# Optimization experiments

Measured on AMD Instinct MI355X. Metric: run time of the kernel, lower is better.

## Reference

```python
import jax, jax.numpy as jnp
import numpy as np

EPS = 1e-5


def _bn_silu(x, gamma, beta):
    # train-mode BatchNorm2d (biased batch stats over N,H,W) followed by SiLU
    m = jnp.mean(x, axis=(0, 2, 3), keepdims=True)
    v = jnp.var(x, axis=(0, 2, 3), keepdims=True)
    y = gamma[None, :, None, None] * (x - m) * jax.lax.rsqrt(v + EPS) + beta[None, :, None, None]
    return y * jax.nn.sigmoid(y)


def _deform_conv2d(x, offset, w, b):
    # x: [B,C,H,W]; offset: [B,2*9,H,W] as (dy,dx) pairs per 3x3 tap; w: [Co,C,3,3]
    B, C, H, W = x.shape
    Co = w.shape[0]
    off = offset.reshape(B, 9, 2, H, W)
    k = jnp.arange(9)
    ky = (k // 3 - 1).astype(x.dtype)  # kernel tap offsets, pad=1 so centered
    kx = (k % 3 - 1).astype(x.dtype)
    py = jnp.arange(H, dtype=x.dtype)[None, None, :, None] + ky[None, :, None, None] + off[:, :, 0]
    px = jnp.arange(W, dtype=x.dtype)[None, None, None, :] + kx[None, :, None, None] + off[:, :, 1]
    y0 = jnp.floor(py)
    x0 = jnp.floor(px)
    wy1 = py - y0
    wx1 = px - x0
    xf = x.reshape(B, C, H * W)

    def corner(yi, xi, cw):
        # zero-padded bilinear corner: mask out-of-bounds taps via weight
        valid = (yi >= 0) & (yi < H) & (xi >= 0) & (xi < W)
        idx = jnp.clip(yi, 0, H - 1) * W + jnp.clip(xi, 0, W - 1)
        g = jnp.take_along_axis(xf, idx.reshape(B, 1, -1), axis=2).reshape(B, C, 9, H, W)
        return g * (cw * valid.astype(x.dtype))[:, None]

    y0i = y0.astype(jnp.int32)
    x0i = x0.astype(jnp.int32)
    s = corner(y0i, x0i, (1 - wy1) * (1 - wx1))
    s = s + corner(y0i, x0i + 1, (1 - wy1) * wx1)
    s = s + corner(y0i + 1, x0i, wy1 * (1 - wx1))
    s = s + corner(y0i + 1, x0i + 1, wy1 * wx1)
    out = jnp.einsum('bckhw,ock->bohw', s, w.reshape(Co, C, 9))
    return out + b[None, :, None, None]


def _conv_transpose(x, w, stride, pad):
    # torch ConvTranspose2d: weight layout [Cin, Cout, kh, kw]
    k = w.shape[2]
    wf = jnp.flip(w, (2, 3)).transpose(1, 0, 2, 3)  # -> OIHW, spatially flipped
    p = k - 1 - pad
    return jax.lax.conv_general_dilated(
        x, wf, (1, 1), [(p, p), (p, p)], lhs_dilation=(stride, stride),
        dimension_numbers=('NCHW', 'OIHW', 'NCHW'))


def setup_inputs() -> dict:
    key = jax.random.key(0)
    ks = jax.random.split(key, 4)
    B, C, Co, H, W = 16, 256, 256, 32, 32
    r = lambda k, s, sc: jax.random.normal(k, s, jnp.float32) * sc
    return {
        'x': r(ks[0], (B, C, H, W), 1.0),
        'w_off': r(ks[1], (18, C, 3, 3), 0.01),
        'b_off': jnp.zeros((18,), jnp.float32),
        'w_def': r(ks[2], (Co, C, 3, 3), 0.02),
        'b_def': jnp.zeros((Co,), jnp.float32),
        'gamma1': jnp.ones((Co,), jnp.float32),
        'beta1': jnp.zeros((Co,), jnp.float32),
        'w_dc': r(ks[3], (Co, Co, 4, 4), 0.02),
        'gamma2': jnp.ones((Co,), jnp.float32),
        'beta2': jnp.zeros((Co,), jnp.float32),
    }


def reference(x, w_off, b_off, w_def, b_def, gamma1, beta1, w_dc, gamma2, beta2):
    offset = jax.lax.conv_general_dilated(
        x, w_off, (1, 1), [(1, 1), (1, 1)],
        dimension_numbers=('NCHW', 'OIHW', 'NCHW')) + b_off[None, :, None, None]
    y = _deform_conv2d(x, offset, w_def, b_def)
    y = _bn_silu(y, gamma1, beta1)
    y = _conv_transpose(y, w_dc, 2, 1)
    return _bn_silu(y, gamma2, beta2)
```

## Files before the change

### kernel.cpp

```cpp
#include <hip/hip_runtime.h>
#include <math.h>

#ifdef __has_builtin
#if __has_builtin(__builtin_amdgcn_global_load_lds)
#define HAS_GLL 1
#endif
#endif
#ifndef HAS_GLL
#define HAS_GLL 0
#endif

typedef __attribute__((ext_vector_type(8))) short short8v;
typedef __attribute__((ext_vector_type(4))) float float4v;

__device__ __forceinline__ unsigned short f2bf(float f) {
    unsigned int u = __float_as_uint(f);
    u += 0x7fffu + ((u >> 16) & 1u);
    return (unsigned short)(u >> 16);
}

__device__ __forceinline__ float silu(float y) { return y / (1.f + expf(-y)); }

__device__ __forceinline__ void stage1k(const void* gsrc, void* ldsbase) {
#if HAS_GLL
    __builtin_amdgcn_global_load_lds((const __attribute__((address_space(1))) unsigned int*)gsrc,
                                     (__attribute__((address_space(3))) unsigned int*)ldsbase,
                                     16, 0, 0);
#else
    int lane = threadIdx.x & 63;
    *(float4*)((char*)ldsbase + lane * 16) = *(const float4*)gsrc;
#endif
}

__global__ __launch_bounds__(256) void k_prep_xt(const float* __restrict__ x,
                                                 unsigned short* __restrict__ xT) {
    int hw0 = blockIdx.x * 32, c0 = blockIdx.y * 32, b = blockIdx.z;
    int t = threadIdx.x;
    __shared__ unsigned short tl[32][36];
    {
        int c_l = t >> 3, w4 = (t & 7) * 4;
        float4 v = *(const float4*)&x[(size_t)((b * 256 + c0 + c_l) * 1024) + hw0 + w4];
        tl[c_l][w4 + 0] = f2bf(v.x);
        tl[c_l][w4 + 1] = f2bf(v.y);
        tl[c_l][w4 + 2] = f2bf(v.z);
        tl[c_l][w4 + 3] = f2bf(v.w);
    }
    __syncthreads();
    {
        int hw_l = t >> 3, c4 = (t & 7) * 4;
        unsigned int s0 = tl[c4 + 0][hw_l];
        unsigned int s1 = tl[c4 + 1][hw_l];
        unsigned int s2 = tl[c4 + 2][hw_l];
        unsigned int s3 = tl[c4 + 3][hw_l];
        uint2 pk;
        pk.x = s0 | (s1 << 16);
        pk.y = s2 | (s3 << 16);
        *(uint2*)&xT[(size_t)((b * 1024 + hw0 + hw_l) * 256) + c0 + c4] = pk;
    }
}

__global__ void k_prep_aoff(const float* __restrict__ w_off, unsigned short* __restrict__ A2off) {
    int i = blockIdx.x * 256 + threadIdx.x;
    int slot = i & 31;
    int oc = (i >> 5) & 31;
    int rest = i >> 10;
    int tap = rest % 9;
    int cc8 = rest / 9;
    int cgrp = (slot >> 3) ^ ((oc >> 1) & 3);
    int c = cc8 * 32 + (cgrp << 3) + (slot & 7);
    unsigned short v = 0;
    if (oc < 18) v = f2bf(w_off[(size_t)oc * 2304 + c * 9 + tap]);
    A2off[i] = v;
}

__global__ void k_prep_a1(const float* __restrict__ w_def, unsigned short* __restrict__ A1) {
    int i = blockIdx.x * 256 + threadIdx.x;
    A1[i] = f2bf(w_def[i]);
}

__global__ void k_prep_a2(const float* __restrict__ w_dc, unsigned short* __restrict__ A2) {
    int i = blockIdx.x * 256 + threadIdx.x;
    int ci = i & 255;
    int tq = (i >> 8) & 3;
    int co = (i >> 10) & 255;
    int p  = i >> 18;
    int ph = p >> 1, pw = p & 1;
    int ty = tq >> 1, tx = tq & 1;
    int kh = 2 * ty + 1 - ph;
    int kw = 2 * tx + 1 - pw;
    A2[i] = f2bf(w_dc[((ci * 256 + co) * 4 + kh) * 4 + kw]);
}

__global__ __launch_bounds__(256) void k_off_gemm(const unsigned short* __restrict__ A2off,
                                                  const unsigned short* __restrict__ xT,
                                                  const float* __restrict__ b_off,
                                                  float* __restrict__ off) {
    int hp = blockIdx.x, b = blockIdx.y;
    int h0 = hp * 2;
    int t = threadIdx.x;
    int lane = t & 63, wid = t >> 6;
    int l15 = lane & 15, g = lane >> 4;
    int swg = (l15 >> 1) & 3;
    __shared__ __align__(16) unsigned short As[9 * 32 * 32];
    __shared__ __align__(16) unsigned short Bsx[4 * 34 * 32];
    float4v acc[2];
    float4v z = {0.f, 0.f, 0.f, 0.f};
    acc[0] = z; acc[1] = z;

    int pos = wid * 16 + l15;
    int py = pos >> 5, px = pos & 31;

    for (int cc8 = 0; cc8 < 8; ++cc8) {
        __syncthreads();
        for (int idx = t; idx < 1152; idx += 256)
            stage1k(A2off + (size_t)cc8 * 9216 + idx * 8, (char*)As + idx * 16);
        for (int idx = t; idx < 544; idx += 256) {
            int r = idx / 136;
            int rem = idx - r * 136;
            int col = rem >> 2;
            int sgrp = rem & 3;
            int grp = sgrp ^ ((col >> 1) & 3);
            int h = h0 - 1 + r;
            int w = col - 1;
            uint4 v = {0u, 0u, 0u, 0u};
            if (h >= 0 && h < 32 && w >= 0 && w < 32)
                v = *(const uint4*)&xT[(size_t)((b * 1024 + h * 32 + w) * 256) + cc8 * 32 + grp * 8];
            *(uint4*)((char*)Bsx + ((r * 34 + col) << 6) + (sgrp << 4)) = v;
        }
        __syncthreads();
#pragma unroll
        for (int tap = 0; tap < 9; ++tap) {
            int ky = tap / 3, kx = tap - ky * 3;
            int col = px + kx;
            int rowr = py + ky;
            short8v bbf = *(const short8v*)((const char*)Bsx + ((rowr * 34 + col) << 6) +
                                            ((g ^ ((col >> 1) & 3)) << 4));
            short8v a0 = *(const short8v*)((const char*)As + tap * 2048 + l15 * 64 + ((g ^ swg) << 4));
            short8v a1 = *(const short8v*)((const char*)As + tap * 2048 + (16 + l15) * 64 + ((g ^ swg) << 4));
            acc[0] = __builtin_amdgcn_mfma_f32_16x16x32_bf16(a0, bbf, acc[0], 0, 0, 0);
            acc[1] = __builtin_amdgcn_mfma_f32_16x16x32_bf16(a1, bbf, acc[1], 0, 0, 0);
        }
    }
    int h = h0 + py;
#pragma unroll
    for (int r = 0; r < 4; ++r) {
        int oc = g * 4 + r;
        off[((size_t)(b * 18 + oc) << 10) + (h << 5) + px] = acc[0][r] + b_off[oc];
    }
    if (g == 0) {
#pragma unroll
        for (int r = 0; r < 2; ++r) {
            int oc = 16 + r;
            off[((size_t)(b * 18 + oc) << 10) + (h << 5) + px] = acc[1][r] + b_off[oc];
        }
    }
}

__global__ __launch_bounds__(576) void k_sample(const float* __restrict__ x,
                                                const float* __restrict__ off,
                                                unsigned short* __restrict__ S) {
    int cg = blockIdx.x, b = blockIdx.y, half = blockIdx.z;
    int cbase = cg * 8;
    int t = threadIdx.x;
    int k = t >> 6, lane = t & 63;
    __shared__ __align__(16) unsigned int xpl[4 * 1156];
    __shared__ __align__(16) unsigned short sS[72 * 66];

    for (int u = t; u < 1024; u += 576) {
        int p = u >> 8, row = (u >> 3) & 31, cq = (u & 7) << 2;
        const float* src0 = x + ((size_t)(b * 256 + cbase + 2 * p) << 10) + (row << 5) + cq;
        float4 a = *(const float4*)src0;
        float4 c = *(const float4*)(src0 + 1024);
        uint4 pk;
        pk.x = (unsigned int)f2bf(a.x) | ((unsigned int)f2bf(c.x) << 16);
        pk.y = (unsigned int)f2bf(a.y) | ((unsigned int)f2bf(c.y) << 16);
        pk.z = (unsigned int)f2bf(a.z) | ((unsigned int)f2bf(c.z) << 16);
        pk.w = (unsigned int)f2bf(a.w) | ((unsigned int)f2bf(c.w) << 16);
        *(uint4*)&xpl[p * 1156 + row * 36 + cq] = pk;
    }

    int wr_row = t / 9, wr_q = t - wr_row * 9;
    const float* offk0 = off + ((size_t)(b * 18 + 2 * k) << 10);
    const float* offk1 = off + ((size_t)(b * 18 + 2 * k + 1) << 10);
    int ky = k / 3 - 1, kx = k % 3 - 1;
    __syncthreads();

    for (int ci = 0; ci < 8; ++ci) {
        int chunk = half * 8 + ci;
        int pos = chunk * 64 + lane;
        int h = pos >> 5, w = pos & 31;
        float dy = offk0[pos];
        float dx = offk1[pos];
        float py = (float)(h + ky) + dy;
        float px = (float)(w + kx) + dx;
        float fy = floorf(py), fx = floorf(px);
        int y0i = (int)fy, x0i = (int)fx;
        float wy = py - fy, wxf = px - fx;
        float vy0 = (y0i >= 0 && y0i < 32) ? 1.f : 0.f;
        float vy1 = (y0i >= -1 && y0i < 31) ? 1.f : 0.f;
        float vx0 = (x0i >= 0 && x0i < 32) ? 1.f : 0.f;
        float vx1 = (x0i >= -1 && x0i < 31) ? 1.f : 0.f;
        int y0c = min(max(y0i, 0), 31), y1c = min(max(y0i + 1, 0), 31);
        int x0c = min(max(x0i, 0), 31), x1c = min(max(x0i + 1, 0), 31);
        float w00 = (1.f - wy) * (1.f - wxf) * vy0 * vx0;
        float w01 = (1.f - wy) * wxf * vy0 * vx1;
        float w10 = wy * (1.f - wxf) * vy1 * vx0;
        float w11 = wy * wxf * vy1 * vx1;
        int a00 = y0c * 36 + x0c, a01 = y0c * 36 + x1c;
        int a10 = y1c * 36 + x0c, a11 = y1c * 36 + x1c;
#pragma unroll
        for (int p = 0; p < 4; ++p) {
            const unsigned int* pl = xpl + p * 1156;
            unsigned int c00 = pl[a00], c01 = pl[a01], c10 = pl[a10], c11 = pl[a11];
            float e00 = __uint_as_float(c00 << 16), o00 = __uint_as_float(c00 & 0xFFFF0000u);
            float e01 = __uint_as_float(c01 << 16), o01 = __uint_as_float(c01 & 0xFFFF0000u);
            float e10 = __uint_as_float(c10 << 16), o10 = __uint_as_float(c10 & 0xFFFF0000u);
            float e11 = __uint_as_float(c11 << 16), o11 = __uint_as_float(c11 & 0xFFFF0000u);
            float ve = w00 * e00 + w01 * e01 + w10 * e10 + w11 * e11;
            float vo = w00 * o00 + w01 * o01 + w10 * o10 + w11 * o11;
            sS[((2 * p) * 9 + k) * 66 + lane] = f2bf(ve);
            sS[((2 * p + 1) * 9 + k) * 66 + lane] = f2bf(vo);
        }
        __syncthreads();
        {
            int basekc = wr_q * 8;
            unsigned int s0 = sS[(basekc + 0) * 66 + wr_row];
            unsigned int s1 = sS[(basekc + 1) * 66 + wr_row];
            unsigned int s2 = sS[(basekc + 2) * 66 + wr_row];
            unsigned int s3 = sS[(basekc + 3) * 66 + wr_row];
            unsigned int s4 = sS[(basekc + 4) * 66 + wr_row];
            unsigned int s5 = sS[(basekc + 5) * 66 + wr_row];
            unsigned int s6 = sS[(basekc + 6) * 66 + wr_row];
            unsigned int s7 = sS[(basekc + 7) * 66 + wr_row];
            uint4 qv;
            qv.x = s0 | (s1 << 16);
            qv.y = s2 | (s3 << 16);
            qv.z = s4 | (s5 << 16);
            qv.w = s6 | (s7 << 16);
            *(uint4*)(S + (size_t)(b * 1024 + chunk * 64 + wr_row) * 2304 + cg * 72 + wr_q * 8) = qv;
        }
        __syncthreads();
    }
}

__global__ __launch_bounds__(256) void k_gemm1(const unsigned short* __restrict__ A1,
                                               const unsigned short* __restrict__ S,
                                               const float* __restrict__ b_def,
                                               float* __restrict__ y1) {
    int nb = blockIdx.x, mb = blockIdx.y;
    int t = threadIdx.x;
    int lane = t & 63, wid = t >> 6;
    int wm = wid >> 1, wn = wid & 1;
    __shared__ __align__(16) unsigned short As[128 * 32];
    __shared__ __align__(16) unsigned short Bs[64 * 32];
    int m0 = mb * 128, n0 = nb * 64;
    float4v acc[4][2];
    float4v z = {0.f, 0.f, 0.f, 0.f};
#pragma unroll
    for (int i = 0; i < 4; ++i) { acc[i][0] = z; acc[i][1] = z; }
    int rQ = lane >> 2;
    int qA = (lane & 3) ^ ((lane >> 3) & 3);
    const unsigned short* gA0 = A1 + (size_t)(m0 + wid * 32 + rQ) * 2304 + qA * 8;
    const unsigned short* gA1 = gA0 + (size_t)16 * 2304;
    const unsigned short* gB0 = S + (size_t)(n0 + wid * 16 + rQ) * 2304 + qA * 8;
    unsigned short* lA0 = As + wid * 32 * 32;
    unsigned short* lA1 = As + (wid * 32 + 16) * 32;
    unsigned short* lB0 = Bs + wid * 16 * 32;
    int g = lane >> 4, l15 = lane & 15;
    int gs = (g ^ ((l15 >> 1) & 3)) << 4;
    for (int s = 0; s < 72; ++s) {
        __syncthreads();
        stage1k(gA0 + s * 32, lA0);
        stage1k(gA1 + s * 32, lA1);
        stage1k(gB0 + s * 32, lB0);
        __syncthreads();
        short8v a[4], bb[2];
#pragma unroll
        for (int mi = 0; mi < 4; ++mi)
            a[mi] = *(const short8v*)((const char*)As + ((wm * 64 + mi * 16 + l15) * 64 + gs));
#pragma unroll
        for (int ni = 0; ni < 2; ++ni)
            bb[ni] = *(const short8v*)((const char*)Bs + ((wn * 32 + ni * 16 + l15) * 64 + gs));
#pragma unroll
        for (int mi = 0; mi < 4; ++mi)
#pragma unroll
            for (int ni = 0; ni < 2; ++ni)
                acc[mi][ni] = __builtin_amdgcn_mfma_f32_16x16x32_bf16(a[mi], bb[ni], acc[mi][ni], 0, 0, 0);
    }
    int b = n0 >> 10;
    int posb = n0 & 1023;
#pragma unroll
    for (int mi = 0; mi < 4; ++mi) {
#pragma unroll
        for (int r = 0; r < 4; ++r) {
            int co = m0 + wm * 64 + mi * 16 + g * 4 + r;
            float bv = b_def[co];
            float* dst = y1 + ((size_t)(b * 256 + co) << 10) + posb;
#pragma unroll
            for (int ni = 0; ni < 2; ++ni)
                dst[wn * 32 + ni * 16 + l15] = acc[mi][ni][r] + bv;
        }
    }
}

__global__ __launch_bounds__(256) void k_gemm2(const unsigned short* __restrict__ A2,
                                               const unsigned short* __restrict__ y1T,
                                               float* __restrict__ outP,
                                               float* __restrict__ pstats2) {
    int nb = blockIdx.x, mb = blockIdx.y, p = blockIdx.z;
    int ph = p >> 1, pw = p & 1;
    int t = threadIdx.x;
    int lane = t & 63, wid = t >> 6;
    int wm = wid >> 1, wn = wid & 1;
    int l15 = lane & 15, g = lane >> 4;
    __shared__ __align__(16) unsigned short As[128 * 64];
    __shared__ __align__(16) unsigned short Bs[128 * 64];
    int m0 = mb * 128, n0 = nb * 128;
    int b = n0 >> 10, pos0 = n0 & 1023, oh0 = pos0 >> 5;

    int dtab[4];
#pragma unroll
    for (int tap = 0; tap < 4; ++tap) {
        int ty = tap >> 1, tx = tap & 1;
        int dy = ph ? (1 - ty) : (-ty);
        int dx = pw ? (1 - tx) : (-tx);
        dtab[tap] = (dy * 34 + dx) * 256;
    }
    const unsigned short* srcA[4];
    const unsigned short* srcB[4];
    unsigned short* dstA[4];
    unsigned short* dstB[4];
#pragma unroll
    for (int it = 0; it < 4; ++it) {
        int idx = t + it * 256;
        int r = idx >> 3, s8 = idx & 7, c = s8 ^ (r & 7);
        srcA[it] = A2 + (size_t)(p * 256 + m0 + r) * 1024 + c * 8;
        dstA[it] = As + idx * 8;
        int ih = oh0 + (r >> 5) + 1;
        int iw = (r & 31) + 1;
        srcB[it] = y1T + ((size_t)(b * 34 + ih) * 34 + iw) * 256 + c * 8;
        dstB[it] = Bs + idx * 8;
    }

    float4v acc[4][4];
    float4v z = {0.f, 0.f, 0.f, 0.f};
#pragma unroll
    for (int i = 0; i < 4; ++i)
#pragma unroll
        for (int j = 0; j < 4; ++j) acc[i][j] = z;

    for (int step = 0; step < 16; ++step) {
        int tap = step >> 2;
        int koff = step * 64;
        int boff = dtab[tap] + (step & 3) * 64;
        __syncthreads();
#pragma unroll
        for (int it = 0; it < 4; ++it) {
            stage1k(srcA[it] + koff, dstA[it]);
            stage1k(srcB[it] + boff, dstB[it]);
        }
        __syncthreads();
#pragma unroll
        for (int kk = 0; kk < 2; ++kk) {
            short8v a[4], bb[4];
#pragma unroll
            for (int mi = 0; mi < 4; ++mi) {
                int row = wm * 64 + mi * 16 + l15;
                int slot = ((kk << 2) + g) ^ (row & 7);
                a[mi] = *(const short8v*)((const char*)As + row * 128 + slot * 16);
            }
#pragma unroll
            for (int ni = 0; ni < 4; ++ni) {
                int row = wn * 64 + ni * 16 + l15;
                int slot = ((kk << 2) + g) ^ (row & 7);
                bb[ni] = *(const short8v*)((const char*)Bs + row * 128 + slot * 16);
            }
#pragma unroll
            for (int mi = 0; mi < 4; ++mi)
#pragma unroll
                for (int ni = 0; ni < 4; ++ni)
                    acc[mi][ni] = __builtin_amdgcn_mfma_f32_16x16x32_bf16(a[mi], bb[ni], acc[mi][ni], 0, 0, 0);
        }
    }
#pragma unroll
    for (int mi = 0; mi < 4; ++mi) {
#pragma unroll
        for (int r = 0; r < 4; ++r) {
            int co = m0 + wm * 64 + mi * 16 + g * 4 + r;
            float* dst = outP + ((size_t)((p * 16 + b) * 256 + co) << 10) + pos0;
#pragma unroll
            for (int ni = 0; ni < 4; ++ni)
                dst[wn * 64 + ni * 16 + l15] = acc[mi][ni][r];
        }
    }
    __syncthreads();
    float* sred  = (float*)As;
    float* s2red = sred + 256;
#pragma unroll
    for (int mi = 0; mi < 4; ++mi) {
#pragma unroll
        for (int r = 0; r < 4; ++r) {
            float s = 0.f, s2 = 0.f;
#pragma unroll
            for (int ni = 0; ni < 4; ++ni) {
                float v = acc[mi][ni][r];
                s += v;
                s2 += v * v;
            }
#pragma unroll
            for (int m = 8; m >= 1; m >>= 1) {
                s  += __shfl_xor(s, m, 64);
                s2 += __shfl_xor(s2, m, 64);
            }
            if (l15 == 0) {
                int col = wm * 64 + mi * 16 + g * 4 + r;
                sred[col * 2 + wn]  = s;
                s2red[col * 2 + wn] = s2;
            }
        }
    }
    __syncthreads();
    if (t < 128) {
        float s  = sred[t * 2] + sred[t * 2 + 1];
        float s2 = s2red[t * 2] + s2red[t * 2 + 1];
        int row = p * 128 + nb;
        int ch = mb * 128 + t;
        pstats2[ch * 512 + row] = s;
        pstats2[131072 + ch * 512 + row] = s2;
    }
}

__global__ __launch_bounds__(256) void k_bnstats_part(const float* __restrict__ src, int nparts,
                                                      float* __restrict__ pstats) {
    int ch = blockIdx.x, j = blockIdx.y;
    int t = threadIdx.x;
    const float* p = src + ((size_t)(j * 256 + ch) << 10);
    float4 v = *(const float4*)&p[t * 4];
    float s  = v.x + v.y + v.z + v.w;
    float s2 = v.x * v.x + v.y * v.y + v.z * v.z + v.w * v.w;
    __shared__ float rs[256], rs2[256];
    rs[t] = s; rs2[t] = s2;
    __syncthreads();
    for (int d = 128; d > 0; d >>= 1) {
        if (t < d) { rs[t] += rs[t + d]; rs2[t] += rs2[t + d]; }
        __syncthreads();
    }
    if (t == 0) {
        pstats[ch * nparts + j] = rs[0];
        pstats[256 * nparts + ch * nparts + j] = rs2[0];
    }
}

__global__ __launch_bounds__(256) void k_bnfin(const float* __restrict__ pstats, int nparts, float n,
                                               float* __restrict__ mean, float* __restrict__ rstd) {
    int ch = threadIdx.x;
    float s = 0.f, s2 = 0.f;
    for (int j = 0; j < nparts; ++j) {
        s += pstats[ch * nparts + j];
        s2 += pstats[256 * nparts + ch * nparts + j];
    }
    float m = s / n;
    float var = s2 / n - m * m;
    mean[ch] = m;
    rstd[ch] = rsqrtf(var + 1e-5f);
}

__global__ __launch_bounds__(256) void k_bnfin2(const float* __restrict__ pstats2,
                                                float* __restrict__ mean, float* __restrict__ rstd) {
    int ch = blockIdx.x;
    int t = threadIdx.x;
    float s  = pstats2[ch * 512 + t] + pstats2[ch * 512 + 256 + t];
    float s2 = pstats2[131072 + ch * 512 + t] + pstats2[131072 + ch * 512 + 256 + t];
    __shared__ float rs[256], rs2[256];
    rs[t] = s; rs2[t] = s2;
    __syncthreads();
    for (int d = 128; d > 0; d >>= 1) {
        if (t < d) { rs[t] += rs[t + d]; rs2[t] += rs2[t + d]; }
        __syncthreads();
    }
    if (t == 0) {
        float n = 65536.f;
        float m = rs[0] / n;
        float var = rs2[0] / n - m * m;
        mean[ch] = m;
        rstd[ch] = rsqrtf(var + 1e-5f);
    }
}

__global__ __launch_bounds__(256) void k_bnsilu_padT(const float* __restrict__ y1,
                                                     const float* __restrict__ mean,
                                                     const float* __restrict__ rstd,
                                                     const float* __restrict__ gamma,
                                                     const float* __restrict__ beta,
                                                     unsigned short* __restrict__ y1T) {
    int py = blockIdx.x, cg = blockIdx.y, b = blockIdx.z;
    int c0 = cg * 32;
    int t = threadIdx.x;
    __shared__ unsigned short tl[32][36];
    {
        int c_l = t >> 3, px4 = (t & 7) * 4;
        int ch = c0 + c_l;
        float m = mean[ch], rs = rstd[ch], ga = gamma[ch], be = beta[ch];
        float4 v = *(const float4*)&y1[(size_t)((b * 256 + ch) << 10) + (py << 5) + px4];
        tl[c_l][px4 + 0] = f2bf(silu(ga * (v.x - m) * rs + be));
        tl[c_l][px4 + 1] = f2bf(silu(ga * (v.y - m) * rs + be));
        tl[c_l][px4 + 2] = f2bf(silu(ga * (v.z - m) * rs + be));
        tl[c_l][px4 + 3] = f2bf(silu(ga * (v.w - m) * rs + be));
    }
    __syncthreads();
    {
        int px = t >> 3, c4 = (t & 7) * 4;
        unsigned int s0 = tl[c4 + 0][px];
        unsigned int s1 = tl[c4 + 1][px];
        unsigned int s2 = tl[c4 + 2][px];
        unsigned int s3 = tl[c4 + 3][px];
        uint2 pk;
        pk.x = s0 | (s1 << 16);
        pk.y = s2 | (s3 << 16);
        *(uint2*)&y1T[((size_t)(b * 34 + py + 1) * 34 + (px + 1)) * 256 + c0 + c4] = pk;
    }
}

__global__ __launch_bounds__(256) void k_bnsilu_out(const float* __restrict__ outP,
                                                    const float* __restrict__ mean,
                                                    const float* __restrict__ rstd,
                                                    const float* __restrict__ gamma,
                                                    const float* __restrict__ beta,
                                                    float* __restrict__ out) {
    unsigned int i = blockIdx.x * 256 + threadIdx.x;
    int ow4 = i & 15;
    int oh = (i >> 4) & 63;
    int co = (i >> 10) & 255;
    int b  = i >> 18;
    int p0 = (oh & 1) * 2;
    int pos = ((oh >> 1) << 5) + ow4 * 2;
    const float* pl0 = outP + ((size_t)((p0 * 16 + b) * 256 + co) << 10) + pos;
    const float* pl1 = pl0 + ((size_t)16 * 256 << 10);
    float2 e = *(const float2*)pl0;
    float2 o = *(const float2*)pl1;
    float m = mean[co], rs = rstd[co], ga = gamma[co], be = beta[co];
    float4 v;
    v.x = silu(ga * (e.x - m) * rs + be);
    v.y = silu(ga * (o.x - m) * rs + be);
    v.z = silu(ga * (e.y - m) * rs + be);
    v.w = silu(ga * (o.y - m) * rs + be);
    *(float4*)&out[((size_t)(b * 256 + co) << 12) + (oh << 6) + ow4 * 4] = v;
}

extern "C" void kernel_launch(void* const* d_in, const int* in_sizes, int n_in,
                              void* d_out, int out_size, void* d_ws, size_t ws_size,
                              hipStream_t stream) {
    const float* x      = (const float*)d_in[0];
    const float* w_off  = (const float*)d_in[1];
    const float* b_off  = (const float*)d_in[2];
    const float* w_def  = (const float*)d_in[3];
    const float* b_def  = (const float*)d_in[4];
    const float* gamma1 = (const float*)d_in[5];
    const float* beta1  = (const float*)d_in[6];
    const float* w_dc   = (const float*)d_in[7];
    const float* gamma2 = (const float*)d_in[8];
    const float* beta2  = (const float*)d_in[9];
    float* out = (float*)d_out;

    char* base = (char*)d_ws;
    unsigned short* S    = (unsigned short*)base;
    float*          y1   = (float*)(base + 75497472);
    unsigned short* y1T  = (unsigned short*)(base + 92274688);
    unsigned short* A1   = (unsigned short*)(base + 101744640);
    unsigned short* A2   = (unsigned short*)(base + 102924288);
    float*          off  = (float*)(base + 105021440);
    float*          stats = (float*)(base + 106201088);
    float* mean1 = stats, *rstd1 = stats + 256, *mean2 = stats + 512, *rstd2 = stats + 768;
    float* pstats = off;
    float* pstats2 = off;
    unsigned short* xT    = (unsigned short*)base;
    unsigned short* A2off = (unsigned short*)(base + 8388608);
    float* outP = (float*)base;

    k_prep_a1<<<2304, 256, 0, stream>>>(w_def, A1);
    k_prep_a2<<<4096, 256, 0, stream>>>(w_dc, A2);
    k_prep_aoff<<<288, 256, 0, stream>>>(w_off, A2off);
    k_prep_xt<<<dim3(32, 8, 16), 256, 0, stream>>>(x, xT);
    k_off_gemm<<<dim3(16, 16), 256, 0, stream>>>(A2off, xT, b_off, off);
    k_sample<<<dim3(32, 16, 2), 576, 0, stream>>>(x, off, S);
    k_gemm1<<<dim3(256, 2), 256, 0, stream>>>(A1, S, b_def, y1);
    k_bnstats_part<<<dim3(256, 16), 256, 0, stream>>>(y1, 16, pstats);
    k_bnfin<<<1, 256, 0, stream>>>(pstats, 16, 16384.f, mean1, rstd1);
    hipMemsetAsync(y1T, 0, 9469952, stream);
    k_bnsilu_padT<<<dim3(32, 8, 16), 256, 0, stream>>>(y1, mean1, rstd1, gamma1, beta1, y1T);
    k_gemm2<<<dim3(128, 2, 4), 256, 0, stream>>>(A2, y1T, outP, pstats2);
    k_bnfin2<<<256, 256, 0, stream>>>(pstats2, mean2, rstd2);
    k_bnsilu_out<<<16384, 256, 0, stream>>>(outP, mean2, rstd2, gamma2, beta2, out);
}
```

Baseline: 212.4 us.

## Double-buffer LDS in both GEMMs, enlarge gemm1 tile, fuse BN1 stats into gemm1

Both GEMM kernels now use two LDS buffers, so the next K-slice loads while MFMAs run on the current one, and each step needs one barrier instead of two. gemm1 moves from a 128x64 tile with K=32 to a 128x128 tile with K=64 and the same swizzled layout as gemm2. Its epilogue also computes per-channel partial sums and sums of squares, which removes the separate k_bnstats_part pass over y1. The cost is 64KB of LDS per block, which may lower occupancy, and k_bnfin now reduces 128 partials per channel instead of 16.

```diff
diff --git a/kernel.cpp b/kernel.cpp
--- a/kernel.cpp
+++ b/kernel.cpp
@@ -246,60 +246,114 @@
 __global__ __launch_bounds__(256) void k_gemm1(const unsigned short* __restrict__ A1,
                                                const unsigned short* __restrict__ S,
                                                const float* __restrict__ b_def,
-                                               float* __restrict__ y1) {
+                                               float* __restrict__ y1,
+                                               float* __restrict__ pstats1) {
     int nb = blockIdx.x, mb = blockIdx.y;
     int t = threadIdx.x;
     int lane = t & 63, wid = t >> 6;
     int wm = wid >> 1, wn = wid & 1;
-    __shared__ __align__(16) unsigned short As[128 * 32];
-    __shared__ __align__(16) unsigned short Bs[64 * 32];
-    int m0 = mb * 128, n0 = nb * 64;
-    float4v acc[4][2];
+    int l15 = lane & 15, g = lane >> 4;
+    __shared__ __align__(16) unsigned short As[2][8192];
+    __shared__ __align__(16) unsigned short Bs[2][8192];
+    int m0 = mb * 128, n0 = nb * 128;
+    int b = n0 >> 10, pos0 = n0 & 1023;
+
+    const unsigned short* srcA[4];
+    const unsigned short* srcB[4];
+    int dstoff[4];
+#pragma unroll
+    for (int it = 0; it < 4; ++it) {
+        int idx = t + it * 256;
+        int r = idx >> 3, s8 = idx & 7, c = s8 ^ (r & 7);
+        srcA[it] = A1 + (size_t)(m0 + r) * 2304 + c * 8;
+        srcB[it] = S + (size_t)(n0 + r) * 2304 + c * 8;
+        dstoff[it] = idx * 8;
+    }
+
+    float4v acc[4][4];
     float4v z = {0.f, 0.f, 0.f, 0.f};
 #pragma unroll
-    for (int i = 0; i < 4; ++i) { acc[i][0] = z; acc[i][1] = z; }
-    int rQ = lane >> 2;
-    int qA = (lane & 3) ^ ((lane >> 3) & 3);
-    const unsigned short* gA0 = A1 + (size_t)(m0 + wid * 32 + rQ) * 2304 + qA * 8;
-    const unsigned short* gA1 = gA0 + (size_t)16 * 2304;
-    const unsigned short* gB0 = S + (size_t)(n0 + wid * 16 + rQ) * 2304 + qA * 8;
-    unsigned short* lA0 = As + wid * 32 * 32;
-    unsigned short* lA1 = As + (wid * 32 + 16) * 32;
-    unsigned short* lB0 = Bs + wid * 16 * 32;
-    int g = lane >> 4, l15 = lane & 15;
-    int gs = (g ^ ((l15 >> 1) & 3)) << 4;
-    for (int s = 0; s < 72; ++s) {
+    for (int i = 0; i < 4; ++i)
+#pragma unroll
+        for (int j = 0; j < 4; ++j) acc[i][j] = z;
+
+#pragma unroll
+    for (int it = 0; it < 4; ++it) {
+        stage1k(srcA[it], &As[0][dstoff[it]]);
+        stage1k(srcB[it], &Bs[0][dstoff[it]]);
+    }
+    __syncthreads();
+
+    for (int step = 0; step < 36; ++step) {
+        int cur = step & 1;
+        if (step < 35) {
+            int koff = (step + 1) * 64;
+#pragma unroll
+            for (int it = 0; it < 4; ++it) {
+                stage1k(srcA[it] + koff, &As[cur ^ 1][dstoff[it]]);
+                stage1k(srcB[it] + koff, &Bs[cur ^ 1][dstoff[it]]);
+            }
+        }
+#pragma unroll
+        for (int kk = 0; kk < 2; ++kk) {
+            short8v a[4], bb[4];
+#pragma unroll
+            for (int mi = 0; mi < 4; ++mi) {
+                int row = wm * 64 + mi * 16 + l15;
+                int slot = ((kk << 2) + g) ^ (row & 7);
+                a[mi] = *(const short8v*)((const char*)&As[cur][0] + row * 128 + slot * 16);
+            }
+#pragma unroll
+            for (int ni = 0; ni < 4; ++ni) {
+                int row = wn * 64 + ni * 16 + l15;
+                int slot = ((kk << 2) + g) ^ (row & 7);
+                bb[ni] = *(const short8v*)((const char*)&Bs[cur][0] + row * 128 + slot * 16);
+            }
+#pragma unroll
+            for (int mi = 0; mi < 4; ++mi)
+#pragma unroll
+                for (int ni = 0; ni < 4; ++ni)
+                    acc[mi][ni] = __builtin_amdgcn_mfma_f32_16x16x32_bf16(a[mi], bb[ni], acc[mi][ni], 0, 0, 0);
+        }
         __syncthreads();
-        stage1k(gA0 + s * 32, lA0);
-        stage1k(gA1 + s * 32, lA1);
-        stage1k(gB0 + s * 32, lB0);
-        __syncthreads();
-        short8v a[4], bb[2];
-#pragma unroll
-        for (int mi = 0; mi < 4; ++mi)
-            a[mi] = *(const short8v*)((const char*)As + ((wm * 64 + mi * 16 + l15) * 64 + gs));
-#pragma unroll
-        for (int ni = 0; ni < 2; ++ni)
-            bb[ni] = *(const short8v*)((const char*)Bs + ((wn * 32 + ni * 16 + l15) * 64 + gs));
-#pragma unroll
-        for (int mi = 0; mi < 4; ++mi)
-#pragma unroll
-            for (int ni = 0; ni < 2; ++ni)
-                acc[mi][ni] = __builtin_amdgcn_mfma_f32_16x16x32_bf16(a[mi], bb[ni], acc[mi][ni], 0, 0, 0);
-    }
-    int b = n0 >> 10;
-    int posb = n0 & 1023;
+    }
+
+    float* sred  = (float*)&As[0][0];
+    float* s2red = sred + 256;
 #pragma unroll
     for (int mi = 0; mi < 4; ++mi) {
 #pragma unroll
         for (int r = 0; r < 4; ++r) {
             int co = m0 + wm * 64 + mi * 16 + g * 4 + r;
             float bv = b_def[co];
-            float* dst = y1 + ((size_t)(b * 256 + co) << 10) + posb;
-#pragma unroll
-            for (int ni = 0; ni < 2; ++ni)
-                dst[wn * 32 + ni * 16 + l15] = acc[mi][ni][r] + bv;
-        }
+            float* dst = y1 + ((size_t)(b * 256 + co) << 10) + pos0;
+            float s = 0.f, s2 = 0.f;
+#pragma unroll
+            for (int ni = 0; ni < 4; ++ni) {
+                float v = acc[mi][ni][r] + bv;
+                dst[wn * 64 + ni * 16 + l15] = v;
+                s += v;
+                s2 += v * v;
+            }
+#pragma unroll
+            for (int m = 8; m >= 1; m >>= 1) {
+                s  += __shfl_xor(s, m, 64);
+                s2 += __shfl_xor(s2, m, 64);
+            }
+            if (l15 == 0) {
+                int col = wm * 64 + mi * 16 + g * 4 + r;
+                sred[col * 2 + wn]  = s;
+                s2red[col * 2 + wn] = s2;
+            }
+        }
+    }
+    __syncthreads();
+    if (t < 128) {
+        float s  = sred[t * 2] + sred[t * 2 + 1];
+        float s2 = s2red[t * 2] + s2red[t * 2 + 1];
+        int ch = m0 + t;
+        pstats1[ch * 128 + nb] = s;
+        pstats1[32768 + ch * 128 + nb] = s2;
     }
 }
 
@@ -313,8 +367,8 @@
     int lane = t & 63, wid = t >> 6;
     int wm = wid >> 1, wn = wid & 1;
     int l15 = lane & 15, g = lane >> 4;
-    __shared__ __align__(16) unsigned short As[128 * 64];
-    __shared__ __align__(16) unsigned short Bs[128 * 64];
+    __shared__ __align__(16) unsigned short As[2][8192];
+    __shared__ __align__(16) unsigned short Bs[2][8192];
     int m0 = mb * 128, n0 = nb * 128;
     int b = n0 >> 10, pos0 = n0 & 1023, oh0 = pos0 >> 5;
 
@@ -328,18 +382,16 @@
     }
     const unsigned short* srcA[4];
     const unsigned short* srcB[4];
-    unsigned short* dstA[4];
-    unsigned short* dstB[4];
+    int dstoff[4];
 #pragma unroll
     for (int it = 0; it < 4; ++it) {
         int idx = t + it * 256;
         int r = idx >> 3, s8 = idx & 7, c = s8 ^ (r & 7);
         srcA[it] = A2 + (size_t)(p * 256 + m0 + r) * 1024 + c * 8;
-        dstA[it] = As + idx * 8;
         int ih = oh0 + (r >> 5) + 1;
         int iw = (r & 31) + 1;
         srcB[it] = y1T + ((size_t)(b * 34 + ih) * 34 + iw) * 256 + c * 8;
-        dstB[it] = Bs + idx * 8;
+        dstoff[it] = idx * 8;
     }
 
     float4v acc[4][4];
@@ -349,17 +401,26 @@
 #pragma unroll
         for (int j = 0; j < 4; ++j) acc[i][j] = z;
 
+#pragma unroll
+    for (int it = 0; it < 4; ++it) {
+        stage1k(srcA[it], &As[0][dstoff[it]]);
+        stage1k(srcB[it] + dtab[0], &Bs[0][dstoff[it]]);
+    }
+    __syncthreads();
+
     for (int step = 0; step < 16; ++step) {
-        int tap = step >> 2;
-        int koff = step * 64;
-        int boff = dtab[tap] + (step & 3) * 64;
-        __syncthreads();
-#pragma unroll
-        for (int it = 0; it < 4; ++it) {
-            stage1k(srcA[it] + koff, dstA[it]);
-            stage1k(srcB[it] + boff, dstB[it]);
-        }
-        __syncthreads();
+        int cur = step & 1;
+        if (step < 15) {
+            int ns = step + 1;
+            int tap = ns >> 2;
+            int koff = ns * 64;
+            int boff = dtab[tap] + (ns & 3) * 64;
+#pragma unroll
+            for (int it = 0; it < 4; ++it) {
+                stage1k(srcA[it] + koff, &As[cur ^ 1][dstoff[it]]);
+                stage1k(srcB[it] + boff, &Bs[cur ^ 1][dstoff[it]]);
+            }
+        }
 #pragma unroll
         for (int kk = 0; kk < 2; ++kk) {
             short8v a[4], bb[4];
@@ -367,13 +428,13 @@
             for (int mi = 0; mi < 4; ++mi) {
                 int row = wm * 64 + mi * 16 + l15;
                 int slot = ((kk << 2) + g) ^ (row & 7);
-                a[mi] = *(const short8v*)((const char*)As + row * 128 + slot * 16);
+                a[mi] = *(const short8v*)((const char*)&As[cur][0] + row * 128 + slot * 16);
             }
 #pragma unroll
             for (int ni = 0; ni < 4; ++ni) {
                 int row = wn * 64 + ni * 16 + l15;
                 int slot = ((kk << 2) + g) ^ (row & 7);
-                bb[ni] = *(const short8v*)((const char*)Bs + row * 128 + slot * 16);
+                bb[ni] = *(const short8v*)((const char*)&Bs[cur][0] + row * 128 + slot * 16);
             }
 #pragma unroll
             for (int mi = 0; mi < 4; ++mi)
@@ -381,6 +442,7 @@
                 for (int ni = 0; ni < 4; ++ni)
                     acc[mi][ni] = __builtin_amdgcn_mfma_f32_16x16x32_bf16(a[mi], bb[ni], acc[mi][ni], 0, 0, 0);
         }
+        __syncthreads();
     }
 #pragma unroll
     for (int mi = 0; mi < 4; ++mi) {
@@ -393,8 +455,7 @@
                 dst[wn * 64 + ni * 16 + l15] = acc[mi][ni][r];
         }
     }
-    __syncthreads();
-    float* sred  = (float*)As;
+    float* sred  = (float*)&As[0][0];
     float* s2red = sred + 256;
 #pragma unroll
     for (int mi = 0; mi < 4; ++mi) {
@@ -424,30 +485,9 @@
         float s  = sred[t * 2] + sred[t * 2 + 1];
         float s2 = s2red[t * 2] + s2red[t * 2 + 1];
         int row = p * 128 + nb;
-        int ch = mb * 128 + t;
+        int ch = m0 + t;
         pstats2[ch * 512 + row] = s;
         pstats2[131072 + ch * 512 + row] = s2;
-    }
-}
-
-__global__ __launch_bounds__(256) void k_bnstats_part(const float* __restrict__ src, int nparts,
-                                                      float* __restrict__ pstats) {
-    int ch = blockIdx.x, j = blockIdx.y;
-    int t = threadIdx.x;
-    const float* p = src + ((size_t)(j * 256 + ch) << 10);
-    float4 v = *(const float4*)&p[t * 4];
-    float s  = v.x + v.y + v.z + v.w;
-    float s2 = v.x * v.x + v.y * v.y + v.z * v.z + v.w * v.w;
-    __shared__ float rs[256], rs2[256];
-    rs[t] = s; rs2[t] = s2;
-    __syncthreads();
-    for (int d = 128; d > 0; d >>= 1) {
-        if (t < d) { rs[t] += rs[t + d]; rs2[t] += rs2[t + d]; }
-        __syncthreads();
-    }
-    if (t == 0) {
-        pstats[ch * nparts + j] = rs[0];
-        pstats[256 * nparts + ch * nparts + j] = rs2[0];
     }
 }
 
@@ -571,7 +611,7 @@
     float*          off  = (float*)(base + 105021440);
     float*          stats = (float*)(base + 106201088);
     float* mean1 = stats, *rstd1 = stats + 256, *mean2 = stats + 512, *rstd2 = stats + 768;
-    float* pstats = off;
+    float* pstats1 = off;
     float* pstats2 = off;
     unsigned short* xT    = (unsigned short*)base;
     unsigned short* A2off = (unsigned short*)(base + 8388608);
@@ -583,9 +623,8 @@
     k_prep_xt<<<dim3(32, 8, 16), 256, 0, stream>>>(x, xT);
     k_off_gemm<<<dim3(16, 16), 256, 0, stream>>>(A2off, xT, b_off, off);
     k_sample<<<dim3(32, 16, 2), 576, 0, stream>>>(x, off, S);
-    k_gemm1<<<dim3(256, 2), 256, 0, stream>>>(A1, S, b_def, y1);
-    k_bnstats_part<<<dim3(256, 16), 256, 0, stream>>>(y1, 16, pstats);
-    k_bnfin<<<1, 256, 0, stream>>>(pstats, 16, 16384.f, mean1, rstd1);
+    k_gemm1<<<dim3(128, 2), 256, 0, stream>>>(A1, S, b_def, y1, pstats1);
+    k_bnfin<<<1, 256, 0, stream>>>(pstats1, 128, 16384.f, mean1, rstd1);
     hipMemsetAsync(y1T, 0, 9469952, stream);
     k_bnsilu_padT<<<dim3(32, 8, 16), 256, 0, stream>>>(y1, mean1, rstd1, gamma1, beta1, y1T);
     k_gemm2<<<dim3(128, 2, 4), 256, 0, stream>>>(A2, y1T, outP, pstats2);
```

Result: slower. 244.8 us (+15.3%).
